# Performance work log

Hardware: AMD Instinct MI355X
Metric: run time of the kernel (lower is better)

The kernel has to match this reference:

```python
import jax, jax.numpy as jnp
import numpy as np

B, S, E = 4, 1024, 768
H, HD = 8, 96  # heads, head_dim (E = H*HD)


def setup_inputs() -> dict:
    key = jax.random.key(0)
    ks = jax.random.split(key, 32)
    init = lambda k, shape: jax.random.normal(k, shape, jnp.float32) * 0.02
    d = {
        'sequence_features': jax.random.normal(ks[0], (B, S, E), jnp.float32),
        # backbone_network: Linear(E,E) ReLU Dropout Linear(E,E)
        'bb_w1': init(ks[1], (E, E)), 'bb_b1': init(ks[2], (E,)),
        'bb_w2': init(ks[3], (E, E)), 'bb_b2': init(ks[4], (E,)),
        # side_chain_network: Linear(E,E//2) ReLU Dropout Linear(E//2,E)
        'sc_w1': init(ks[5], (E, E // 2)), 'sc_b1': init(ks[6], (E // 2,)),
        'sc_w2': init(ks[7], (E // 2, E)), 'sc_b2': init(ks[8], (E,)),
        # contact predictor: MultiheadAttention(E, 8) + MLP(E->384->1)
        'attn_wq': init(ks[9], (E, E)), 'attn_bq': init(ks[10], (E,)),
        'attn_wk': init(ks[11], (E, E)), 'attn_bk': init(ks[12], (E,)),
        'attn_wv': init(ks[13], (E, E)), 'attn_bv': init(ks[14], (E,)),
        'attn_wo': init(ks[15], (E, E)), 'attn_bo': init(ks[16], (E,)),
        'mlp_w1': init(ks[17], (E, 384)), 'mlp_b1': init(ks[18], (384,)),
        'mlp_w2': init(ks[19], (384, 1)), 'mlp_b2': init(ks[20], (1,)),
        # structure refiner processors
        'rb_w1': init(ks[21], (E, 384)), 'rb_b1': init(ks[22], (384,)),
        'rb_w2': init(ks[23], (384, 3)), 'rb_b2': init(ks[24], (3,)),
        'rs_w1': init(ks[25], (E, 384)), 'rs_b1': init(ks[26], (384,)),
        'rs_w2': init(ks[27], (384, 4)), 'rs_b2': init(ks[28], (4,)),
    }
    return d


def _pdist(s):
    # batched pairwise euclidean distances with torch-cdist-like zero-grad at d=0
    xx = jnp.sum(s * s, axis=-1)
    d2 = xx[:, :, None] + xx[:, None, :] - 2.0 * jnp.einsum('bid,bjd->bij', s, s)
    d2 = jnp.maximum(d2, 0.0)
    safe = jnp.sqrt(jnp.where(d2 > 0, d2, 1.0))
    return jnp.where(d2 > 0, safe, 0.0)


def reference(sequence_features, bb_w1, bb_b1, bb_w2, bb_b2, sc_w1, sc_b1, sc_w2, sc_b2,
              attn_wq, attn_bq, attn_wk, attn_bk, attn_wv, attn_bv, attn_wo, attn_bo,
              mlp_w1, mlp_b1, mlp_w2, mlp_b2, rb_w1, rb_b1, rb_w2, rb_b2,
              rs_w1, rs_b1, rs_w2, rs_b2):
    x = sequence_features  # [B,S,E]
    # backbone / side-chain feature networks (dropout = identity at eval)
    backbone = jax.nn.relu(x @ bb_w1 + bb_b1) @ bb_w2 + bb_b2            # [B,S,E]
    side = jax.nn.relu(backbone @ sc_w1 + sc_b1) @ sc_w2 + sc_b2        # [B,S,E]

    # --- ContactMapPredictor ---
    # torch MHA default batch_first=False: input [B,S,E] is treated as (L=B, N=S, E),
    # i.e. attention runs OVER THE BATCH AXIS. Faithfully reproduced.
    q = (x @ attn_wq + attn_bq).reshape(B, S, H, HD)
    k = (x @ attn_wk + attn_bk).reshape(B, S, H, HD)
    v = (x @ attn_wv + attn_bv).reshape(B, S, H, HD)
    scores = jnp.einsum('bshd,cshd->shbc', q, k) / jnp.sqrt(jnp.float32(HD))
    attn = jax.nn.softmax(scores, axis=-1)
    ao = jnp.einsum('shbc,cshd->bshd', attn, v).reshape(B, S, E) @ attn_wo + attn_bo
    probs = jax.nn.relu(ao @ mlp_w1 + mlp_b1) @ mlp_w2 + mlp_b2          # [B,S,1]
    # contacts[:, i, :] = probs[:, i] broadcast over last axis
    contacts = jnp.broadcast_to(probs, (B, S, S))

    # --- StructureRefiner ---
    ba = jax.nn.relu(backbone @ rb_w1 + rb_b1) @ rb_w2 + rb_b2           # [B,S,3]
    sa = jax.nn.relu(side @ rs_w1 + rs_b1) @ rs_w2 + rs_b2               # [B,S,4], computed but unused (as in source)
    del sa
    phi, psi = ba[..., 0], ba[..., 1]  # omega unused in source
    steps = 3.8 * jnp.stack([jnp.cos(phi) * jnp.cos(psi),
                             jnp.sin(phi) * jnp.cos(psi),
                             jnp.sin(psi)], axis=-1)                      # [B,S,3]
    steps = steps.at[:, 0].set(0.0)  # structure[:,0] stays at origin
    structure = jnp.cumsum(steps, axis=1)  # the serial i-loop is a cumsum

    def loss_fn(s):
        dists = _pdist(s)
        contact_loss = jnp.mean(jnp.abs(dists - 8.0) * contacts)
        diag = jnp.diagonal(dists, axis1=1, axis2=2)
        chain_loss = jnp.mean(jnp.abs(diag - 3.8))
        return contact_loss + chain_loss

    lr, beta1, beta2, eps = 0.01, 0.9, 0.999, 1e-8

    def adam_step(carry, t):
        s, m, v = carry
        g = jax.grad(loss_fn)(s)
        m = beta1 * m + (1.0 - beta1) * g
        v = beta2 * v + (1.0 - beta2) * g * g
        mhat = m / (1.0 - beta1 ** t)
        vhat = v / (1.0 - beta2 ** t)
        s = s - lr * mhat / (jnp.sqrt(vhat) + eps)
        return (s, m, v), None

    ts = jnp.arange(1, 51, dtype=jnp.float32)
    (structure, _, _), _ = jax.lax.scan(
        adam_step, (structure, jnp.zeros_like(structure), jnp.zeros_like(structure)), ts)
    structure = jax.lax.stop_gradient(structure)  # .detach() in source

    return backbone, side, contacts, structure
```

## Files before the change

### kernel.cpp

```cpp
#include <hip/hip_runtime.h>
#include <cmath>

static constexpr int Bb = 4, Ss = 1024, Ee = 768, Hh = 8, HDd = 96;
static constexpr int BS = Bb * Ss;
static constexpr size_t SLOT_EF = (size_t)BS * Ee;

typedef __attribute__((ext_vector_type(8))) short short8v;
typedef __attribute__((ext_vector_type(4))) float f32x4;

__device__ __forceinline__ ushort f2b(float f) {
    unsigned u = __float_as_uint(f);
    return (ushort)((u + 0x7FFFu + ((u >> 16) & 1u)) >> 16);
}
__device__ __forceinline__ float b2f(ushort b) {
    return __uint_as_float(((unsigned)b) << 16);
}
__device__ __forceinline__ void gload16(const void* g, void* l) {
    __builtin_amdgcn_global_load_lds(
        (const __attribute__((address_space(1))) unsigned int*)g,
        (__attribute__((address_space(3))) unsigned int*)l, 16, 0, 0);
}

__global__ __launch_bounds__(256) void cvt_bf16_k(
    const float* __restrict__ in, ushort* __restrict__ out, int n)
{
    const int i = (blockIdx.x * 256 + threadIdx.x) * 4;
    if (i >= n) return;
    const float4 v = *reinterpret_cast<const float4*>(in + i);
    ushort4 o;
    o.x = f2b(v.x); o.y = f2b(v.y); o.z = f2b(v.z); o.w = f2b(v.w);
    *reinterpret_cast<ushort4*>(out + i) = o;
}

struct TDesc { const float* src; ushort* dst; int K; int N; int tile0; };
struct TPack { TDesc e[10]; };

__global__ __launch_bounds__(256) void tcvt_multi_k(TPack p)
{
    __shared__ float tile[64][65];
    const int tb = blockIdx.x;
    int idx = 0;
#pragma unroll
    for (int i = 1; i < 10; ++i) if (tb >= p.e[i].tile0) idx = i;
    const TDesc d = p.e[idx];
    const int lt = tb - d.tile0;
    const int ntn = d.N >> 6;
    const int nb = (lt % ntn) << 6;
    const int kb = (lt / ntn) << 6;
    const int t = threadIdx.x;
    {
        const int nn = t & 63, k4 = t >> 6;
#pragma unroll
        for (int r = 0; r < 16; ++r) {
            const int kk = (k4 << 4) + r;
            tile[kk][nn] = d.src[(size_t)(kb + kk) * d.N + nb + nn];
        }
    }
    __syncthreads();
    {
        const int kk = t & 63, n4 = t >> 6;
#pragma unroll
        for (int r = 0; r < 16; ++r) {
            const int nn = (n4 << 4) + r;
            d.dst[(size_t)(nb + nn) * d.K + kb + kk] = f2b(tile[kk][nn]);
        }
    }
}

__global__ __launch_bounds__(256) void concat_bias_k(
    const float* __restrict__ a, const float* __restrict__ b,
    const float* __restrict__ c, float* __restrict__ o)
{
    const int i = blockIdx.x * 256 + threadIdx.x;
    if (i < 768) o[i] = a[i];
    else if (i < 1536) o[i] = b[i - 768];
    else if (i < 2304) o[i] = c[i - 1536];
}

template <int RELU, int WF32, int WB16>
__global__ __launch_bounds__(256) void gemm_bf16_k(
    const ushort* __restrict__ A, const ushort* __restrict__ Bt,
    const float* __restrict__ bias,
    float* __restrict__ Cf, ushort* __restrict__ Cb,
    int M, int N, int K)
{
    __shared__ ushort As[128 * 32];
    __shared__ ushort Bs[128 * 32];
    const int t = threadIdx.x, lane = t & 63, wid = t >> 6;
    const int bm = blockIdx.y, bn = blockIdx.x;
    const int wr = wid >> 1, wc = wid & 1;

    const int r0 = wid * 32 + (lane >> 2);
    const int sc = (lane & 3) * 8;
    const ushort* Ag0 = A  + (size_t)(bm * 128 + r0) * K + sc;
    const ushort* Ag1 = Ag0 + (size_t)16 * K;
    const ushort* Bg0 = Bt + (size_t)(bn * 128 + r0) * K + sc;
    const ushort* Bg1 = Bg0 + (size_t)16 * K;
    char* AsB = (char*)As + wid * 2048;
    char* BsB = (char*)Bs + wid * 2048;

    f32x4 acc[4][4];
#pragma unroll
    for (int m = 0; m < 4; ++m)
#pragma unroll
        for (int n = 0; n < 4; ++n) acc[m][n] = (f32x4){0.f, 0.f, 0.f, 0.f};

    const int fr = lane & 15, ks = (lane >> 4) * 8;

    for (int k0 = 0; k0 < K; k0 += 32) {
        __syncthreads();
        gload16(Ag0 + k0, AsB);
        gload16(Ag1 + k0, AsB + 1024);
        gload16(Bg0 + k0, BsB);
        gload16(Bg1 + k0, BsB + 1024);
        __syncthreads();

        short8v a[4], b[4];
#pragma unroll
        for (int m = 0; m < 4; ++m)
            a[m] = *reinterpret_cast<const short8v*>(&As[(wr * 64 + m * 16 + fr) * 32 + ks]);
#pragma unroll
        for (int n = 0; n < 4; ++n)
            b[n] = *reinterpret_cast<const short8v*>(&Bs[(wc * 64 + n * 16 + fr) * 32 + ks]);
#pragma unroll
        for (int m = 0; m < 4; ++m)
#pragma unroll
            for (int n = 0; n < 4; ++n)
                acc[m][n] = __builtin_amdgcn_mfma_f32_16x16x32_bf16(a[m], b[n], acc[m][n], 0, 0, 0);
    }

    const int col0 = bn * 128 + wc * 64 + (lane & 15);
    const int rw0  = bm * 128 + wr * 64 + (lane >> 4) * 4;
#pragma unroll
    for (int n = 0; n < 4; ++n) {
        const int col = col0 + n * 16;
        const float bv = bias[col];
#pragma unroll
        for (int m = 0; m < 4; ++m) {
            const f32x4 v = acc[m][n];
#pragma unroll
            for (int r = 0; r < 4; ++r) {
                const int row = rw0 + m * 16 + r;
                float val = v[r] + bv;
                if (RELU) val = fmaxf(val, 0.f);
                if (WF32) Cf[(size_t)row * N + col] = val;
                if (WB16) Cb[(size_t)row * N + col] = f2b(val);
            }
        }
    }
}

__global__ __launch_bounds__(256) void attn_wave_k(
    const ushort* __restrict__ qkv, ushort* __restrict__ ao)
{
    const int wv = (blockIdx.x << 2) + (threadIdx.x >> 6);
    const int lane = threadIdx.x & 63;
    const int s = wv >> 3, h = wv & 7;
    const int c0 = h * HDd;
    const bool has2 = lane < 32;

    float qq[4][2], kk[4][2];
#pragma unroll
    for (int b = 0; b < 4; ++b) {
        const size_t base = (size_t)(b * Ss + s) * 2304 + c0;
        qq[b][0] = b2f(qkv[base + lane]);
        qq[b][1] = has2 ? b2f(qkv[base + 64 + lane]) : 0.f;
        kk[b][0] = b2f(qkv[base + 768 + lane]);
        kk[b][1] = has2 ? b2f(qkv[base + 768 + 64 + lane]) : 0.f;
    }
    float sc[4][4];
#pragma unroll
    for (int b = 0; b < 4; ++b)
#pragma unroll
        for (int c = 0; c < 4; ++c)
            sc[b][c] = qq[b][0] * kk[c][0] + qq[b][1] * kk[c][1];
#pragma unroll
    for (int msk = 1; msk < 64; msk <<= 1)
#pragma unroll
        for (int b = 0; b < 4; ++b)
#pragma unroll
            for (int c = 0; c < 4; ++c)
                sc[b][c] += __shfl_xor(sc[b][c], msk, 64);

    const float scale = 0.10206207261596577f;
    float at[4][4];
#pragma unroll
    for (int b = 0; b < 4; ++b) {
        const float mx = fmaxf(fmaxf(sc[b][0], sc[b][1]), fmaxf(sc[b][2], sc[b][3]));
        float sum = 0.f;
#pragma unroll
        for (int c = 0; c < 4; ++c) { at[b][c] = expf((sc[b][c] - mx) * scale); sum += at[b][c]; }
        const float inv = 1.f / sum;
#pragma unroll
        for (int c = 0; c < 4; ++c) at[b][c] *= inv;
    }

    float vv[4][2];
#pragma unroll
    for (int c = 0; c < 4; ++c) {
        const size_t base = (size_t)(c * Ss + s) * 2304 + 1536 + c0;
        vv[c][0] = b2f(qkv[base + lane]);
        vv[c][1] = has2 ? b2f(qkv[base + 64 + lane]) : 0.f;
    }
#pragma unroll
    for (int b = 0; b < 4; ++b) {
        float o0 = 0.f, o1 = 0.f;
#pragma unroll
        for (int c = 0; c < 4; ++c) { o0 = fmaf(at[b][c], vv[c][0], o0); o1 = fmaf(at[b][c], vv[c][1], o1); }
        const size_t obase = (size_t)(b * Ss + s) * Ee + c0;
        ao[obase + lane] = f2b(o0);
        if (has2) ao[obase + 64 + lane] = f2b(o1);
    }
}

__global__ __launch_bounds__(256) void mlp2_probs_k(
    const float* __restrict__ m1, const float* __restrict__ w2,
    const float* __restrict__ b2, float* __restrict__ probs)
{
    const int gid = blockIdx.x * 256 + threadIdx.x;
    const int row = gid >> 6, lane = gid & 63;
    if (row >= BS) return;
    float acc = 0.f;
    for (int kk = lane; kk < 384; kk += 64)
        acc = fmaf(m1[(size_t)row * 384 + kk], w2[kk], acc);
#pragma unroll
    for (int off = 32; off > 0; off >>= 1) acc += __shfl_down(acc, off, 64);
    if (lane == 0) probs[row] = acc + b2[0];
}

__global__ __launch_bounds__(256) void rb2_ba_k(
    const float* __restrict__ r1, const float* __restrict__ w2,
    const float* __restrict__ b2, float* __restrict__ ba)
{
    const int gid = blockIdx.x * 256 + threadIdx.x;
    const int row = gid >> 6, lane = gid & 63;
    if (row >= BS) return;
    float a0 = 0.f, a1 = 0.f, a2 = 0.f;
    for (int kk = lane; kk < 384; kk += 64) {
        const float r = r1[(size_t)row * 384 + kk];
        a0 = fmaf(r, w2[kk * 3 + 0], a0);
        a1 = fmaf(r, w2[kk * 3 + 1], a1);
        a2 = fmaf(r, w2[kk * 3 + 2], a2);
    }
#pragma unroll
    for (int off = 32; off > 0; off >>= 1) {
        a0 += __shfl_down(a0, off, 64);
        a1 += __shfl_down(a1, off, 64);
        a2 += __shfl_down(a2, off, 64);
    }
    if (lane == 0) {
        ba[(size_t)row * 3 + 0] = a0 + b2[0];
        ba[(size_t)row * 3 + 1] = a1 + b2[1];
        ba[(size_t)row * 3 + 2] = a2 + b2[2];
    }
}

__global__ __launch_bounds__(256) void contacts_k(
    const float* __restrict__ probs, float* __restrict__ out)
{
    const int f4 = blockIdx.x * 256 + threadIdx.x;
    if (f4 >= (Bb * Ss * Ss) / 4) return;
    const int row = f4 >> 8;
    const float p = probs[row];
    reinterpret_cast<float4*>(out)[f4] = make_float4(p, p, p, p);
}

__global__ __launch_bounds__(1024) void steps_cumsum_k(
    const float* __restrict__ ba, float* __restrict__ sPad)
{
    const int b = blockIdx.x;
    const int i = threadIdx.x;
    const int row = b * Ss + i;
    const float phi = ba[(size_t)row * 3 + 0];
    const float psi = ba[(size_t)row * 3 + 1];
    const float cpsi = cosf(psi);
    float x = 3.8f * cosf(phi) * cpsi;
    float y = 3.8f * sinf(phi) * cpsi;
    float z = 3.8f * sinf(psi);
    if (i == 0) { x = 0.f; y = 0.f; z = 0.f; }
    __shared__ float sx[1024], sy[1024], sz[1024];
    sx[i] = x; sy[i] = y; sz[i] = z;
    for (int off = 1; off < 1024; off <<= 1) {
        __syncthreads();
        float ax = 0.f, ay = 0.f, az = 0.f;
        if (i >= off) { ax = sx[i - off]; ay = sy[i - off]; az = sz[i - off]; }
        __syncthreads();
        sx[i] += ax; sy[i] += ay; sz[i] += az;
    }
    *reinterpret_cast<float4*>(sPad + ((size_t)row << 2)) = make_float4(sx[i], sy[i], sz[i], 0.f);
}

__global__ __launch_bounds__(512) void adam_coop7_k(
    float* __restrict__ sA, float* __restrict__ sB, float* __restrict__ outS,
    const float* __restrict__ probs, unsigned* flags)
{
    const int tid = threadIdx.x, lane = tid & 63, wv = tid >> 6;
    const int bk = blockIdx.x;
    const int batch = bk >> 6;
    const int jbase = batch << 10;
    const int lr = (bk & 63) * 16 + wv * 2;
    const int rbase = jbase + lr;
    unsigned* fb = flags + (batch << 6);

    __shared__ float sx[1024], sy[1024], sz[1024], pSh[1024];
    for (int i = tid; i < 1024; i += 512) pSh[i] = probs[jbase + i];

    float m[2][3] = {}, v[2][3] = {};
    float pb1 = 1.f, pb2 = 1.f;
    const float invN = 1.f / 4194304.f;

    for (int t = 1; t <= 50; ++t) {
        const float* rbuf = (t & 1) ? sA : sB;
        float* wbuf = (t & 1) ? sB : sA;
        for (int r = tid; r < 1024; r += 512) {
            const float* p = rbuf + (((size_t)(jbase + r)) << 2);
            const unsigned long long xy = __hip_atomic_load(
                (const unsigned long long*)p, __ATOMIC_RELAXED, __HIP_MEMORY_SCOPE_AGENT);
            const float zz = __hip_atomic_load(p + 2, __ATOMIC_RELAXED, __HIP_MEMORY_SCOPE_AGENT);
            sx[r] = __uint_as_float((unsigned)xy);
            sy[r] = __uint_as_float((unsigned)(xy >> 32));
            sz[r] = zz;
        }
        __syncthreads();

        pb1 *= 0.9f; pb2 *= 0.999f;
        const float bc1 = 1.f / (1.f - pb1);
        const float bc2 = 1.f / (1.f - pb2);

        float srx[2], sry[2], srz[2], pr[2], g[2][3] = {};
#pragma unroll
        for (int r = 0; r < 2; ++r) {
            srx[r] = sx[lr + r]; sry[r] = sy[lr + r]; srz[r] = sz[lr + r]; pr[r] = pSh[lr + r];
        }

        for (int it = 0; it < 16; ++it) {
            const int j = it * 64 + lane;
            const float qx = sx[j], qy = sy[j], qz = sz[j];
            const float pj = pSh[j];
#pragma unroll
            for (int r = 0; r < 2; ++r) {
                const float dx = srx[r] - qx, dy = sry[r] - qy, dz = srz[r] - qz;
                const float d2 = dx * dx + dy * dy + dz * dz;
                if (d2 > 0.f) {
                    const float w = ((d2 > 64.f) ? 1.f : -1.f) * (pr[r] + pj) * rsqrtf(d2);
                    g[r][0] = fmaf(w, dx, g[r][0]);
                    g[r][1] = fmaf(w, dy, g[r][1]);
                    g[r][2] = fmaf(w, dz, g[r][2]);
                }
            }
        }
#pragma unroll
        for (int msk = 1; msk < 64; msk <<= 1)
#pragma unroll
            for (int r = 0; r < 2; ++r)
#pragma unroll
                for (int c = 0; c < 3; ++c)
                    g[r][c] += __shfl_xor(g[r][c], msk, 64);

        float ns[2][3];
#pragma unroll
        for (int r = 0; r < 2; ++r) {
            const float sc_[3] = { srx[r], sry[r], srz[r] };
#pragma unroll
            for (int c = 0; c < 3; ++c) {
                const float gg = g[r][c] * invN;
                m[r][c] = 0.9f * m[r][c] + 0.1f * gg;
                v[r][c] = 0.999f * v[r][c] + 0.001f * gg * gg;
                ns[r][c] = sc_[c] - 0.01f * (m[r][c] * bc1) / (sqrtf(v[r][c] * bc2) + 1e-8f);
            }
        }

        if (t == 50) {
            if (lane == 0) {
#pragma unroll
                for (int r = 0; r < 2; ++r)
#pragma unroll
                    for (int c = 0; c < 3; ++c)
                        outS[(size_t)(rbase + r) * 3 + c] = ns[r][c];
            }
            return;
        }

        if (lane == 0) {
#pragma unroll
            for (int r = 0; r < 2; ++r) {
                float* dst = wbuf + (((size_t)(rbase + r)) << 2);
                const unsigned long long xy =
                    ((unsigned long long)__float_as_uint(ns[r][1]) << 32)
                    | (unsigned long long)__float_as_uint(ns[r][0]);
                __hip_atomic_store((unsigned long long*)dst, xy,
                                   __ATOMIC_RELAXED, __HIP_MEMORY_SCOPE_AGENT);
                __hip_atomic_store(dst + 2, ns[r][2],
                                   __ATOMIC_RELAXED, __HIP_MEMORY_SCOPE_AGENT);
            }
        }
        __syncthreads();
        if (tid == 0)
            __hip_atomic_store(&fb[bk & 63], (unsigned)t,
                               __ATOMIC_RELEASE, __HIP_MEMORY_SCOPE_AGENT);
        if (wv == 0) {
            for (;;) {
                const unsigned f = __hip_atomic_load(&fb[lane], __ATOMIC_RELAXED,
                                                     __HIP_MEMORY_SCOPE_AGENT);
                if (__all(f >= (unsigned)t)) break;
                __builtin_amdgcn_s_sleep(1);
            }
        }
        asm volatile("" ::: "memory");
        __syncthreads();
    }
}

extern "C" void kernel_launch(void* const* d_in, const int* in_sizes, int n_in,
                              void* d_out, int out_size, void* d_ws, size_t ws_size,
                              hipStream_t stream)
{
    const float* x     = (const float*)d_in[0];
    const float* bb_w1 = (const float*)d_in[1];
    const float* bb_b1 = (const float*)d_in[2];
    const float* bb_w2 = (const float*)d_in[3];
    const float* bb_b2 = (const float*)d_in[4];
    const float* sc_w1 = (const float*)d_in[5];
    const float* sc_b1 = (const float*)d_in[6];
    const float* sc_w2 = (const float*)d_in[7];
    const float* sc_b2 = (const float*)d_in[8];
    const float* wq_p = (const float*)d_in[9];  const float* bq = (const float*)d_in[10];
    const float* wk_p = (const float*)d_in[11]; const float* bk = (const float*)d_in[12];
    const float* wv_p = (const float*)d_in[13]; const float* bv = (const float*)d_in[14];
    const float* wo_p = (const float*)d_in[15]; const float* bo = (const float*)d_in[16];
    const float* mlp_w1 = (const float*)d_in[17]; const float* mlp_b1 = (const float*)d_in[18];
    const float* mlp_w2 = (const float*)d_in[19]; const float* mlp_b2 = (const float*)d_in[20];
    const float* rb_w1 = (const float*)d_in[21]; const float* rb_b1 = (const float*)d_in[22];
    const float* rb_w2 = (const float*)d_in[23]; const float* rb_b2 = (const float*)d_in[24];

    float* out_backbone = (float*)d_out;
    float* out_side     = out_backbone + SLOT_EF;
    float* out_contacts = out_side + SLOT_EF;
    float* out_struct   = out_contacts + (size_t)Bb * Ss * Ss;

    ushort* cur = (ushort*)d_ws;
    ushort* xb        = cur; cur += SLOT_EF;
    ushort* mb        = cur; cur += SLOT_EF;
    ushort* backboneb = cur; cur += SLOT_EF;
    ushort* s1b       = cur; cur += (size_t)BS * 384;
    ushort* bb_w1t    = cur; cur += 768 * 768;
    ushort* bb_w2t    = cur; cur += 768 * 768;
    ushort* qkvWt     = cur; cur += 2304 * 768;
    ushort* wot       = cur; cur += 768 * 768;
    ushort* sc_w1t    = cur; cur += 768 * 384;
    ushort* sc_w2t    = cur; cur += 768 * 384;
    ushort* mlp_w1t   = cur; cur += 768 * 384;
    ushort* rb_w1t    = cur; cur += 768 * 384;
    float* fcur = (float*)cur;
    float* qkvBias = fcur; fcur += 2304;
    float* probs   = fcur; fcur += BS;
    float* ba      = fcur; fcur += 3 * BS;
    float* sPA     = fcur; fcur += 4 * BS;
    float* sPB     = fcur; fcur += 4 * BS;
    unsigned* flags = (unsigned*)fcur; fcur += 256;

    ushort* qkvb = (ushort*)out_backbone;
    ushort* aob  = (ushort*)out_contacts;
    ushort* h1b  = (ushort*)out_contacts;
    float*  m1f  = out_side + (size_t)BS * 384;
    float*  r1f  = (float*)xb;

    const dim3 blk(256);
    const dim3 gEE(768 / 128, BS / 128);
    const dim3 gEH(384 / 128, BS / 128);
    const dim3 gQKV(2304 / 128, BS / 128);

    cvt_bf16_k<<<dim3((int)(SLOT_EF / 4 / 256)), blk, 0, stream>>>(x, xb, (int)SLOT_EF);
    {
        TPack tp; int t0 = 0; int ti = 0;
        auto add = [&](const float* s, ushort* d, int K, int N) {
            tp.e[ti].src = s; tp.e[ti].dst = d; tp.e[ti].K = K; tp.e[ti].N = N; tp.e[ti].tile0 = t0;
            t0 += (N / 64) * (K / 64); ++ti;
        };
        add(bb_w1, bb_w1t, 768, 768);
        add(bb_w2, bb_w2t, 768, 768);
        add(wq_p, qkvWt,                 768, 768);
        add(wk_p, qkvWt + 768 * 768,     768, 768);
        add(wv_p, qkvWt + 2 * 768 * 768, 768, 768);
        add(wo_p, wot, 768, 768);
        add(sc_w1, sc_w1t, 768, 384);
        add(sc_w2, sc_w2t, 384, 768);
        add(mlp_w1, mlp_w1t, 768, 384);
        add(rb_w1, rb_w1t, 768, 384);
        tcvt_multi_k<<<dim3(t0), blk, 0, stream>>>(tp);
    }
    concat_bias_k<<<dim3(9), blk, 0, stream>>>(bq, bk, bv, qkvBias);

    gemm_bf16_k<0, 0, 1><<<gQKV, blk, 0, stream>>>(xb, qkvWt, qkvBias, nullptr, qkvb, BS, 2304, 768);
    attn_wave_k<<<dim3(Ss * Hh / 4), blk, 0, stream>>>(qkvb, aob);
    gemm_bf16_k<0, 0, 1><<<gEE, blk, 0, stream>>>(aob, wot, bo, nullptr, mb, BS, 768, 768);
    gemm_bf16_k<1, 1, 0><<<gEH, blk, 0, stream>>>(mb, mlp_w1t, mlp_b1, m1f, nullptr, BS, 384, 768);
    mlp2_probs_k<<<dim3(BS * 64 / 256), blk, 0, stream>>>(m1f, mlp_w2, mlp_b2, probs);

    gemm_bf16_k<1, 0, 1><<<gEE, blk, 0, stream>>>(xb, bb_w1t, bb_b1, nullptr, h1b, BS, 768, 768);
    gemm_bf16_k<0, 1, 1><<<gEE, blk, 0, stream>>>(h1b, bb_w2t, bb_b2, out_backbone, backboneb, BS, 768, 768);
    gemm_bf16_k<1, 0, 1><<<gEH, blk, 0, stream>>>(backboneb, sc_w1t, sc_b1, nullptr, s1b, BS, 384, 768);
    gemm_bf16_k<0, 1, 0><<<gEE, blk, 0, stream>>>(s1b, sc_w2t, sc_b2, out_side, nullptr, BS, 768, 384);

    contacts_k<<<dim3(Bb * Ss * Ss / 4 / 256), blk, 0, stream>>>(probs, out_contacts);

    gemm_bf16_k<1, 1, 0><<<gEH, blk, 0, stream>>>(backboneb, rb_w1t, rb_b1, r1f, nullptr, BS, 384, 768);
    rb2_ba_k<<<dim3(BS * 64 / 256), blk, 0, stream>>>(r1f, rb_w2, rb_b2, ba);
    steps_cumsum_k<<<dim3(Bb), dim3(1024), 0, stream>>>(ba, sPA);

    hipMemsetAsync(flags, 0, 256 * sizeof(unsigned), stream);
    {
        void* args[] = { (void*)&sPA, (void*)&sPB, (void*)&out_struct, (void*)&probs,
                         (void*)&flags };
        hipLaunchCooperativeKernel(reinterpret_cast<void*>(adam_coop7_k),
                                   dim3(256), dim3(512), args, 0, stream);
    }
}
```

Before: 682.7 us.

## Replace per-step barrier in Adam loop with per-step flags and incremental consumption

The cooperative Adam kernel no longer waits at a full per-batch barrier every step. Each block publishes a per-step ready flag and triple-buffers positions. Consumers poll the flags and process 64-row groups of the previous step's positions as soon as the four producing blocks for a group are ready, overlapping the gradient work with stragglers. The block's own row positions are kept in registers instead of being reloaded from shared memory. In exchange there are extra __syncthreads per polling round, more flag memory (50 steps x 4 batches x 64), and the correctness of the triple buffer depends on how far blocks can drift apart.

```diff
diff --git a/kernel.cpp b/kernel.cpp
--- a/kernel.cpp
+++ b/kernel.cpp
@@ -290,65 +290,106 @@
     *reinterpret_cast<float4*>(sPad + ((size_t)row << 2)) = make_float4(sx[i], sy[i], sz[i], 0.f);
 }
 
-__global__ __launch_bounds__(512) void adam_coop7_k(
-    float* __restrict__ sA, float* __restrict__ sB, float* __restrict__ outS,
+__global__ __launch_bounds__(512) void adam_pipe_k(
+    const float* __restrict__ sInit, float* __restrict__ b0f, float* __restrict__ b1f,
+    float* __restrict__ b2f, float* __restrict__ outS,
     const float* __restrict__ probs, unsigned* flags)
 {
     const int tid = threadIdx.x, lane = tid & 63, wv = tid >> 6;
     const int bk = blockIdx.x;
     const int batch = bk >> 6;
+    const int sb = bk & 63;
     const int jbase = batch << 10;
-    const int lr = (bk & 63) * 16 + wv * 2;
+    const int lr = sb * 16 + wv * 2;
     const int rbase = jbase + lr;
-    unsigned* fb = flags + (batch << 6);
 
     __shared__ float sx[1024], sy[1024], sz[1024], pSh[1024];
+    __shared__ unsigned gmaskSh;
     for (int i = tid; i < 1024; i += 512) pSh[i] = probs[jbase + i];
 
+    float srx[2], sry[2], srz[2], pr[2];
+#pragma unroll
+    for (int r = 0; r < 2; ++r) {
+        const float4 q = *reinterpret_cast<const float4*>(sInit + (((size_t)(rbase + r)) << 2));
+        srx[r] = q.x; sry[r] = q.y; srz[r] = q.z;
+        pr[r] = probs[rbase + r];
+    }
     float m[2][3] = {}, v[2][3] = {};
     float pb1 = 1.f, pb2 = 1.f;
     const float invN = 1.f / 4194304.f;
+    float* bufs[3] = { b0f, b1f, b2f };
 
     for (int t = 1; t <= 50; ++t) {
-        const float* rbuf = (t & 1) ? sA : sB;
-        float* wbuf = (t & 1) ? sB : sA;
-        for (int r = tid; r < 1024; r += 512) {
-            const float* p = rbuf + (((size_t)(jbase + r)) << 2);
-            const unsigned long long xy = __hip_atomic_load(
-                (const unsigned long long*)p, __ATOMIC_RELAXED, __HIP_MEMORY_SCOPE_AGENT);
-            const float zz = __hip_atomic_load(p + 2, __ATOMIC_RELAXED, __HIP_MEMORY_SCOPE_AGENT);
-            sx[r] = __uint_as_float((unsigned)xy);
-            sy[r] = __uint_as_float((unsigned)(xy >> 32));
-            sz[r] = zz;
-        }
-        __syncthreads();
+        const float* rbuf = (t == 1) ? sInit : bufs[(t - 1) % 3];
+        float* wbuf = bufs[t % 3];
+        const unsigned* flgIn = flags + (((t - 2) * 4 + batch) << 6);
 
         pb1 *= 0.9f; pb2 *= 0.999f;
         const float bc1 = 1.f / (1.f - pb1);
         const float bc2 = 1.f / (1.f - pb2);
 
-        float srx[2], sry[2], srz[2], pr[2], g[2][3] = {};
-#pragma unroll
-        for (int r = 0; r < 2; ++r) {
-            srx[r] = sx[lr + r]; sry[r] = sy[lr + r]; srz[r] = sz[lr + r]; pr[r] = pSh[lr + r];
-        }
-
-        for (int it = 0; it < 16; ++it) {
-            const int j = it * 64 + lane;
-            const float qx = sx[j], qy = sy[j], qz = sz[j];
-            const float pj = pSh[j];
-#pragma unroll
-            for (int r = 0; r < 2; ++r) {
-                const float dx = srx[r] - qx, dy = sry[r] - qy, dz = srz[r] - qz;
-                const float d2 = dx * dx + dy * dy + dz * dz;
-                if (d2 > 0.f) {
-                    const float w = ((d2 > 64.f) ? 1.f : -1.f) * (pr[r] + pj) * rsqrtf(d2);
-                    g[r][0] = fmaf(w, dx, g[r][0]);
-                    g[r][1] = fmaf(w, dy, g[r][1]);
-                    g[r][2] = fmaf(w, dz, g[r][2]);
+        unsigned done = 0;
+        float g[2][3] = {};
+        while (done != 0xFFFFu) {
+            if (wv == 0) {
+                unsigned gm = 0xFFFFu;
+                if (t > 1) {
+                    const unsigned f = __hip_atomic_load(flgIn + lane, __ATOMIC_RELAXED,
+                                                         __HIP_MEMORY_SCOPE_AGENT);
+                    const unsigned long long rdy = __ballot(f != 0u);
+                    gm = 0;
+#pragma unroll
+                    for (int k = 0; k < 16; ++k)
+                        if (((rdy >> (4 * k)) & 0xFull) == 0xFull) gm |= (1u << k);
                 }
-            }
-        }
+                if (lane == 0) gmaskSh = gm;
+            }
+            __syncthreads();
+            const unsigned newg = gmaskSh & ~done;
+            if (newg) {
+#pragma unroll 1
+                for (int gi = 0; gi < 16; ++gi) {
+                    if (((newg >> gi) & 1u) && ((gi & 7) == wv)) {
+                        const int j = (gi << 6) + lane;
+                        const float* p = rbuf + (((size_t)(jbase + j)) << 2);
+                        const unsigned long long xy = __hip_atomic_load(
+                            (const unsigned long long*)p, __ATOMIC_RELAXED,
+                            __HIP_MEMORY_SCOPE_AGENT);
+                        const float zz = __hip_atomic_load(p + 2, __ATOMIC_RELAXED,
+                                                           __HIP_MEMORY_SCOPE_AGENT);
+                        sx[j] = __uint_as_float((unsigned)xy);
+                        sy[j] = __uint_as_float((unsigned)(xy >> 32));
+                        sz[j] = zz;
+                    }
+                }
+            }
+            __syncthreads();
+            if (newg) {
+#pragma unroll 1
+                for (int gi = 0; gi < 16; ++gi) {
+                    if ((newg >> gi) & 1u) {
+                        const int j = (gi << 6) + lane;
+                        const float qx = sx[j], qy = sy[j], qz = sz[j];
+                        const float pj = pSh[j];
+#pragma unroll
+                        for (int r = 0; r < 2; ++r) {
+                            const float dx = srx[r] - qx, dy = sry[r] - qy, dz = srz[r] - qz;
+                            const float d2 = dx * dx + dy * dy + dz * dz;
+                            if (d2 > 0.f) {
+                                const float w = ((d2 > 64.f) ? 1.f : -1.f) * (pr[r] + pj) * rsqrtf(d2);
+                                g[r][0] = fmaf(w, dx, g[r][0]);
+                                g[r][1] = fmaf(w, dy, g[r][1]);
+                                g[r][2] = fmaf(w, dz, g[r][2]);
+                            }
+                        }
+                    }
+                }
+                done |= newg;
+            } else {
+                __builtin_amdgcn_s_sleep(1);
+            }
+        }
+
 #pragma unroll
         for (int msk = 1; msk < 64; msk <<= 1)
 #pragma unroll
@@ -357,26 +398,28 @@
                 for (int c = 0; c < 3; ++c)
                     g[r][c] += __shfl_xor(g[r][c], msk, 64);
 
-        float ns[2][3];
 #pragma unroll
         for (int r = 0; r < 2; ++r) {
+            float ns[3];
             const float sc_[3] = { srx[r], sry[r], srz[r] };
 #pragma unroll
             for (int c = 0; c < 3; ++c) {
                 const float gg = g[r][c] * invN;
                 m[r][c] = 0.9f * m[r][c] + 0.1f * gg;
                 v[r][c] = 0.999f * v[r][c] + 0.001f * gg * gg;
-                ns[r][c] = sc_[c] - 0.01f * (m[r][c] * bc1) / (sqrtf(v[r][c] * bc2) + 1e-8f);
-            }
+                ns[c] = sc_[c] - 0.01f * (m[r][c] * bc1) / (sqrtf(v[r][c] * bc2) + 1e-8f);
+            }
+            srx[r] = ns[0]; sry[r] = ns[1]; srz[r] = ns[2];
         }
 
         if (t == 50) {
             if (lane == 0) {
 #pragma unroll
-                for (int r = 0; r < 2; ++r)
-#pragma unroll
-                    for (int c = 0; c < 3; ++c)
-                        outS[(size_t)(rbase + r) * 3 + c] = ns[r][c];
+                for (int r = 0; r < 2; ++r) {
+                    outS[(size_t)(rbase + r) * 3 + 0] = srx[r];
+                    outS[(size_t)(rbase + r) * 3 + 1] = sry[r];
+                    outS[(size_t)(rbase + r) * 3 + 2] = srz[r];
+                }
             }
             return;
         }
@@ -386,28 +429,18 @@
             for (int r = 0; r < 2; ++r) {
                 float* dst = wbuf + (((size_t)(rbase + r)) << 2);
                 const unsigned long long xy =
-                    ((unsigned long long)__float_as_uint(ns[r][1]) << 32)
-                    | (unsigned long long)__float_as_uint(ns[r][0]);
+                    ((unsigned long long)__float_as_uint(sry[r]) << 32)
+                    | (unsigned long long)__float_as_uint(srx[r]);
                 __hip_atomic_store((unsigned long long*)dst, xy,
                                    __ATOMIC_RELAXED, __HIP_MEMORY_SCOPE_AGENT);
-                __hip_atomic_store(dst + 2, ns[r][2],
+                __hip_atomic_store(dst + 2, srz[r],
                                    __ATOMIC_RELAXED, __HIP_MEMORY_SCOPE_AGENT);
             }
         }
         __syncthreads();
         if (tid == 0)
-            __hip_atomic_store(&fb[bk & 63], (unsigned)t,
+            __hip_atomic_store(flags + (((t - 1) * 4 + batch) << 6) + sb, 1u,
                                __ATOMIC_RELEASE, __HIP_MEMORY_SCOPE_AGENT);
-        if (wv == 0) {
-            for (;;) {
-                const unsigned f = __hip_atomic_load(&fb[lane], __ATOMIC_RELAXED,
-                                                     __HIP_MEMORY_SCOPE_AGENT);
-                if (__all(f >= (unsigned)t)) break;
-                __builtin_amdgcn_s_sleep(1);
-            }
-        }
-        asm volatile("" ::: "memory");
-        __syncthreads();
     }
 }
 
@@ -456,8 +489,10 @@
     float* probs   = fcur; fcur += BS;
     float* ba      = fcur; fcur += 3 * BS;
     float* sPA     = fcur; fcur += 4 * BS;
-    float* sPB     = fcur; fcur += 4 * BS;
-    unsigned* flags = (unsigned*)fcur; fcur += 256;
+    float* rb0     = fcur; fcur += 4 * BS;
+    float* rb1     = fcur; fcur += 4 * BS;
+    float* rb2     = fcur; fcur += 4 * BS;
+    unsigned* flags = (unsigned*)fcur; fcur += 50 * 4 * 64;
 
     ushort* qkvb = (ushort*)out_backbone;
     ushort* aob  = (ushort*)out_contacts;
@@ -508,11 +543,11 @@
     rb2_ba_k<<<dim3(BS * 64 / 256), blk, 0, stream>>>(r1f, rb_w2, rb_b2, ba);
     steps_cumsum_k<<<dim3(Bb), dim3(1024), 0, stream>>>(ba, sPA);
 
-    hipMemsetAsync(flags, 0, 256 * sizeof(unsigned), stream);
+    hipMemsetAsync(flags, 0, (size_t)50 * 4 * 64 * sizeof(unsigned), stream);
     {
-        void* args[] = { (void*)&sPA, (void*)&sPB, (void*)&out_struct, (void*)&probs,
-                         (void*)&flags };
-        hipLaunchCooperativeKernel(reinterpret_cast<void*>(adam_coop7_k),
+        void* args[] = { (void*)&sPA, (void*)&rb0, (void*)&rb1, (void*)&rb2,
+                         (void*)&out_struct, (void*)&probs, (void*)&flags };
+        hipLaunchCooperativeKernel(reinterpret_cast<void*>(adam_pipe_k),
                                    dim3(256), dim3(512), args, 0, stream);
     }
 }
```

Result: slower. 764.9 us (+12.0%).
